# Kernel tuning notes

Hardware: AMD Instinct MI355X
Metric: run time of the kernel (lower is better)

Reference implementation:

```python
import jax, jax.numpy as jnp
import numpy as np
from jax.scipy.linalg import expm

VOCAB = 32000
DM = 256
STATES = (64, 128, 256, 512)
BATCH = 4
SEQ = 1024
RH = 64  # router hidden
NW = len(STATES)


def setup_inputs() -> dict:
    key = jax.random.key(0)
    ks = jax.random.split(key, 32)
    inp = {"x": jax.random.randint(ks[0], (BATCH, SEQ), 0, VOCAB)}
    inp["emb"] = jax.random.normal(ks[1], (VOCAB, DM), jnp.float32)
    for i, ds in enumerate(STATES):
        inp[f"A{i}"] = jax.random.normal(ks[2 + 3 * i], (ds, ds), jnp.float32) * 0.01
        inp[f"B{i}"] = jax.random.normal(ks[3 + 3 * i], (DM, ds), jnp.float32) * 0.01
        inp[f"C{i}"] = jax.random.normal(ks[4 + 3 * i], (ds, DM), jnp.float32) * 0.01
        inp[f"D{i}"] = jnp.ones((DM,), jnp.float32)
    inp["rw1"] = jax.random.normal(ks[20], (DM, RH), jnp.float32) * (1.0 / np.sqrt(DM))
    inp["rb1"] = jnp.zeros((RH,), jnp.float32)
    inp["rw2"] = jax.random.normal(ks[21], (RH, NW), jnp.float32) * (1.0 / np.sqrt(RH))
    inp["rb2"] = jnp.zeros((NW,), jnp.float32)
    inp["ow"] = jax.random.normal(ks[22], (DM, VOCAB), jnp.float32) * (1.0 / np.sqrt(DM))
    inp["ob"] = jnp.zeros((VOCAB,), jnp.float32)
    return inp


def world_ssm(xe, A, B, C, D):
    # xe: [b, s, dm]; LTI recurrence h_t = h_{t-1} @ A_d + x_t @ B; y_t = h_t @ C + x_t * D
    Ad = expm(A * 0.1)
    h0 = jnp.zeros((xe.shape[0], A.shape[0]), xe.dtype)

    def step(h, xt):
        h = h @ Ad + xt @ B
        return h, h @ C + xt * D

    _, ys = jax.lax.scan(step, h0, jnp.swapaxes(xe, 0, 1))  # scan over time
    return jnp.swapaxes(ys, 0, 1)  # [b, s, dm]


def reference(x, emb, A0, B0, C0, D0, A1, B1, C1, D1, A2, B2, C2, D2,
              A3, B3, C3, D3, rw1, rb1, rw2, rb2, ow, ob):
    xe = emb[x]  # [b, s, dm]
    # soft router over worlds from mean-pooled embedding
    w = jax.nn.softmax(jax.nn.relu(xe.mean(axis=1) @ rw1 + rb1) @ rw2 + rb2, axis=-1)  # [b, 4]
    worlds = [(A0, B0, C0, D0), (A1, B1, C1, D1), (A2, B2, C2, D2), (A3, B3, C3, D3)]
    out = jnp.zeros_like(xe)
    for i, p in enumerate(worlds):
        out = out + w[:, i][:, None, None] * world_ssm(xe, *p)
    return out @ ow + ob  # [b, s, vocab]
```

## Files before the change

### kernel.cpp

```cpp
#include <hip/hip_runtime.h>
#include <stdint.h>
#include <string.h>

#define DM 256
#define NB 4
#define SEQ 1024
#define NTOK 4096
#define RHID 64
#define DSUM 960
#define SZ2 348160
#define VOCABN 32000
#define XROWS 6144
#define XPADE (XROWS * DSUM)

typedef __attribute__((ext_vector_type(8))) short short8;
typedef __attribute__((ext_vector_type(4))) float floatx4;

__device__ __forceinline__ unsigned short f2bf(float f) {
  unsigned int x = __float_as_uint(f);
  x += 0x7fffu + ((x >> 16) & 1u);
  return (unsigned short)(x >> 16);
}
__device__ __forceinline__ float bf2f(unsigned short u) {
  return __uint_as_float(((unsigned int)u) << 16);
}

__device__ __forceinline__ void gll16(const unsigned short* g, unsigned short* l) {
  __builtin_amdgcn_global_load_lds((const __attribute__((address_space(1))) void*)g,
                                   (__attribute__((address_space(3))) void*)l, 16, 0, 0);
}

struct Ptr4 { const float* p[4]; };


__global__ void k_embed(const int* x, const float* emb, float* xe, unsigned short* xebf) {
  int r = blockIdx.x;
  int d = threadIdx.x;
  int tok = x[r];
  float v = emb[(size_t)tok * DM + d];
  xe[(size_t)r * DM + d] = v;
  xebf[(size_t)r * DM + d] = f2bf(v);
}

__global__ void k_mean(const float* xe, float* mean) {
  __shared__ float red[4][DM];
  int b = blockIdx.x;
  int tid = threadIdx.x;
  int d = tid & 255, tt = tid >> 8;
  float s = 0.f;
  for (int t = tt; t < SEQ; t += 4) s += xe[((size_t)b * SEQ + t) * DM + d];
  red[tt][d] = s;
  __syncthreads();
  if (tt == 0) mean[b * DM + d] = (red[0][d] + red[1][d] + red[2][d] + red[3][d]) * (1.f / SEQ);
}

__global__ void k_router(const float* mean, const float* rw1, const float* rb1,
                         const float* rw2, const float* rb2, Ptr4 Dv,
                         float* wout, float* wD) {
  __shared__ float r1[4][RHID];
  __shared__ float lg[4][4];
  __shared__ float wsh[4][4];
  int tid = threadIdx.x;
  int b = tid >> 6, h = tid & 63;
  float s = rb1[h];
  for (int d0 = 0; d0 < DM; d0++) s += mean[b * DM + d0] * rw1[d0 * RHID + h];
  r1[b][h] = fmaxf(s, 0.f);
  __syncthreads();
  if (tid < 16) {
    int bb = tid >> 2, i = tid & 3;
    float s2 = rb2[i];
    for (int hh = 0; hh < RHID; hh++) s2 += r1[bb][hh] * rw2[hh * 4 + i];
    lg[bb][i] = s2;
  }
  __syncthreads();
  if (tid < 4) {
    float m = lg[tid][0];
    for (int i = 1; i < 4; i++) m = fmaxf(m, lg[tid][i]);
    float e[4], sum = 0.f;
    for (int i = 0; i < 4; i++) { e[i] = __expf(lg[tid][i] - m); sum += e[i]; }
    for (int i = 0; i < 4; i++) { wsh[tid][i] = e[i] / sum; wout[tid * 4 + i] = wsh[tid][i]; }
  }
  __syncthreads();
  int d = tid;
  for (int bb = 0; bb < 4; bb++) {
    float v = 0.f;
    for (int i = 0; i < 4; i++) v += wsh[bb][i] * Dv.p[i][d];
    wD[bb * DM + d] = v;
  }
}

__device__ __forceinline__ void world_from_id(int id, int& w, int& e) {
  if (id < 4096)        { w = 0; e = id; }
  else if (id < 20480)  { w = 1; e = id - 4096; }
  else if (id < 86016)  { w = 2; e = id - 20480; }
  else                  { w = 3; e = id - 86016; }
}

__global__ void k_prep_M(Ptr4 A, unsigned short* Mh, unsigned short* Ml,
                         unsigned short* MTh, unsigned short* MTl) {
  int id = blockIdx.x * 256 + threadIdx.x;
  int w, e; world_from_id(id, w, e);
  int s = 6 + w, ds = 64 << w;
  int i = e >> s, j = e & (ds - 1);
  float v = 0.1f * A.p[w][e];
  unsigned short h = f2bf(v);
  unsigned short l = f2bf(v - bf2f(h));
  Mh[id] = h; Ml[id] = l;
  int tix = (id - e) + (j << s) + i;
  MTh[tix] = h; MTl[tix] = l;
}

__global__ void k_combine(Ptr4 A, const float* P2f, const float* P3f, const float* P4f,
                          unsigned short* Ph, unsigned short* Pl,
                          unsigned short* PTh, unsigned short* PTl) {
  int id = blockIdx.x * 256 + threadIdx.x;
  int w, e; world_from_id(id, w, e);
  int s = 6 + w, ds = 64 << w;
  int i = e >> s, j = e & (ds - 1);
  float v = ((i == j) ? 1.f : 0.f) + 0.1f * A.p[w][e]
          + 0.5f * P2f[id] + (1.f / 6.f) * P3f[id] + (1.f / 24.f) * P4f[id];
  unsigned short h = f2bf(v);
  unsigned short l = f2bf(v - bf2f(h));
  Ph[id] = h; Pl[id] = l;
  int tix = (id - e) + (j << s) + i;
  PTh[tix] = h; PTl[tix] = l;
}

__global__ void k_prep_B(Ptr4 B, unsigned short* BtCat) {
  int jc = blockIdx.x;
  int d = threadIdx.x;
  int w, j;
  if (jc < 64)       { w = 0; j = jc; }
  else if (jc < 192) { w = 1; j = jc - 64; }
  else if (jc < 448) { w = 2; j = jc - 192; }
  else               { w = 3; j = jc - 448; }
  int ds = 64 << w;
  BtCat[(size_t)jc * DM + d] = f2bf(B.p[w][(size_t)d * ds + j]);
}

__global__ void k_prep_C(Ptr4 C, unsigned short* CtCat) {
  int c = blockIdx.x * 256 + threadIdx.x;
  int d = blockIdx.y;
  if (c >= DSUM) return;
  int w, j;
  if (c < 64)       { w = 0; j = c; }
  else if (c < 192) { w = 1; j = c - 64; }
  else if (c < 448) { w = 2; j = c - 192; }
  else              { w = 3; j = c - 448; }
  CtCat[(size_t)d * DSUM + c] = f2bf(C.p[w][(size_t)j * DM + d]);
}

__global__ void k_transpose_ow(const float* ow, unsigned short* owT) {
  __shared__ float t[64][65];
  int n0 = blockIdx.x * 64, k0 = blockIdx.y * 64;
  int tid = threadIdx.x;
  int a = tid >> 6, b = tid & 63;
  #pragma unroll
  for (int r = 0; r < 16; r++) {
    int k = r * 4 + a;
    t[k][b] = ow[(size_t)(k0 + k) * VOCABN + n0 + b];
  }
  __syncthreads();
  #pragma unroll
  for (int r = 0; r < 16; r++) {
    int n = r * 4 + a;
    owT[(size_t)(n0 + n) * DM + k0 + b] = f2bf(t[b][n]);
  }
}

__global__ void k_zero(uint4* p, long n) {
  long i = (long)blockIdx.x * blockDim.x + threadIdx.x;
  long stride = (long)gridDim.x * blockDim.x;
  uint4 z = make_uint4(0, 0, 0, 0);
  for (; i < n; i += stride) p[i] = z;
}

__global__ void k_finish_op(const float* opf, const float* xe, const float* wD, unsigned short* op) {
  int r = blockIdx.x, dcol = threadIdx.x;
  size_t i = (size_t)r * DM + dcol;
  op[i] = f2bf(opf[i] + xe[i] * wD[(size_t)(r >> 10) * DM + dcol]);
}


struct GDesc {
  const unsigned short *Ah, *Al, *Bth, *Btl;
  float *Cf;
  unsigned short *Ch, *Cl, *Th, *Tl;
  int M, N, K, lda, ldbt, ldc, ldt, split, tn, boff;
};
struct GArgs { GDesc d[4]; int nd; };

__global__ __launch_bounds__(256) void gemm_uni(GArgs ga) {
  int di = ga.nd - 1;
  while (di > 0 && (int)blockIdx.x < ga.d[di].boff) di--;
  const GDesc& d = ga.d[di];
  int lb = blockIdx.x - d.boff;
  int tm = lb / d.tn, tnn = lb % d.tn;
  int m0 = tm * 128, n0 = tnn * 128;

  __shared__ unsigned short As[2][128][40];
  __shared__ unsigned short Bs[2][128][40];

  int tid = threadIdx.x;
  int wave = tid >> 6, lane = tid & 63;
  int wm = (wave >> 1) * 64, wn = (wave & 1) * 64;
  int q = lane >> 4, l15 = lane & 15;

  floatx4 acc[4][4];
  #pragma unroll
  for (int i = 0; i < 4; i++)
    #pragma unroll
    for (int j = 0; j < 4; j++)
      acc[i][j] = (floatx4){0.f, 0.f, 0.f, 0.f};

  for (int kt = 0; kt < d.K; kt += 32) {
    __syncthreads();
    #pragma unroll
    for (int c0 = 0; c0 < 2; c0++) {
      int c = c0 * 256 + tid;
      int row = c >> 2, k8 = (c & 3) << 3;
      {
        int gr = m0 + row;
        uint4 hv = make_uint4(0, 0, 0, 0), lv = make_uint4(0, 0, 0, 0);
        if (gr < d.M) {
          size_t idx = (size_t)gr * d.lda + kt + k8;
          hv = *(const uint4*)(d.Ah + idx);
          if (d.split) lv = *(const uint4*)(d.Al + idx);
        }
        *(uint4*)&As[0][row][k8] = hv;
        if (d.split) *(uint4*)&As[1][row][k8] = lv;
      }
      {
        int gn = n0 + row;
        uint4 hv = make_uint4(0, 0, 0, 0), lv = make_uint4(0, 0, 0, 0);
        if (gn < d.N) {
          size_t idx = (size_t)gn * d.ldbt + kt + k8;
          hv = *(const uint4*)(d.Bth + idx);
          if (d.split) lv = *(const uint4*)(d.Btl + idx);
        }
        *(uint4*)&Bs[0][row][k8] = hv;
        if (d.split) *(uint4*)&Bs[1][row][k8] = lv;
      }
    }
    __syncthreads();
    short8 bh[4], bl[4];
    #pragma unroll
    for (int j = 0; j < 4; j++)
      bh[j] = *(const short8*)&Bs[0][wn + j * 16 + l15][q * 8];
    if (d.split) {
      #pragma unroll
      for (int j = 0; j < 4; j++)
        bl[j] = *(const short8*)&Bs[1][wn + j * 16 + l15][q * 8];
    }
    #pragma unroll
    for (int i = 0; i < 4; i++) {
      short8 ah = *(const short8*)&As[0][wm + i * 16 + l15][q * 8];
      #pragma unroll
      for (int j = 0; j < 4; j++)
        acc[i][j] = __builtin_amdgcn_mfma_f32_16x16x32_bf16(ah, bh[j], acc[i][j], 0, 0, 0);
      if (d.split) {
        short8 al = *(const short8*)&As[1][wm + i * 16 + l15][q * 8];
        #pragma unroll
        for (int j = 0; j < 4; j++) {
          acc[i][j] = __builtin_amdgcn_mfma_f32_16x16x32_bf16(ah, bl[j], acc[i][j], 0, 0, 0);
          acc[i][j] = __builtin_amdgcn_mfma_f32_16x16x32_bf16(al, bh[j], acc[i][j], 0, 0, 0);
        }
      }
    }
  }

  #pragma unroll
  for (int i = 0; i < 4; i++) {
    #pragma unroll
    for (int j = 0; j < 4; j++) {
      int col = n0 + wn + j * 16 + l15;
      if (col >= d.N) continue;
      #pragma unroll
      for (int r = 0; r < 4; r++) {
        int row = m0 + wm + i * 16 + q * 4 + r;
        if (row >= d.M) continue;
        float v = acc[i][j][r];
        size_t ci = (size_t)row * d.ldc + col;
        if (d.Cf) d.Cf[ci] = v;
        if (d.Ch) {
          unsigned short h = f2bf(v);
          d.Ch[ci] = h;
          if (d.Cl) d.Cl[ci] = f2bf(v - bf2f(h));
        }
        if (d.Th) {
          size_t tix = (size_t)col * d.ldt + row;
          unsigned short h = f2bf(v);
          d.Th[tix] = h;
          d.Tl[tix] = f2bf(v - bf2f(h));
        }
      }
    }
  }
}


struct KDesc {
  const unsigned short *Ah, *Al, *Bth, *Btl;
  unsigned short *Ch, *Cl, *Hc;
  const float* wcol;
  int N, K, lda, ldbt, shift, hcoff, tn, boff;
};
struct KArgs { KDesc d[4]; int nd; };

template<int SPLIT, int KS>
__global__ __launch_bounds__(256) void gemm_x(KArgs ga) {
  int di = ga.nd - 1;
  while (di > 0 && (int)blockIdx.x < ga.d[di].boff) di--;
  const KDesc& d = ga.d[di];
  int lb = blockIdx.x - d.boff;
  int tm = lb / d.tn, tnn = lb % d.tn;
  int m0 = tm * 128, n0 = tnn * 128;
  int prow0 = ((m0 >> 10) * 1536) + 512 + (m0 & 1023);
  int arow0 = KS ? (prow0 - d.shift) : m0;

  __shared__ unsigned short As[(SPLIT ? 2 : 1) * 4096];
  __shared__ unsigned short Bs[(SPLIT ? 2 : 1) * 4096];

  int tid = threadIdx.x;
  int wave = tid >> 6, lane = tid & 63;
  int wm = (wave >> 1) * 64, wn = (wave & 1) * 64;
  int q = lane >> 4, l15 = lane & 15;
  int srow = lane >> 2, scol = (lane & 3) * 8;

  floatx4 acc[4][4];
  #pragma unroll
  for (int i = 0; i < 4; i++)
    #pragma unroll
    for (int j = 0; j < 4; j++)
      acc[i][j] = (floatx4){0.f, 0.f, 0.f, 0.f};

  for (int kt = 0; kt < d.K; kt += 32) {
    int ar = arow0 + wave * 32 + srow;
    int br = n0 + wave * 32 + srow;
    const unsigned short* ag = d.Ah + (size_t)ar * d.lda + kt + scol;
    const unsigned short* bg = d.Bth + (size_t)br * d.ldbt + kt + scol;
    size_t as16 = (size_t)16 * d.lda, bs16 = (size_t)16 * d.ldbt;
    unsigned short* al0 = &As[wave * 32 * 32];
    unsigned short* bl0 = &Bs[wave * 32 * 32];
    gll16(ag, al0);        gll16(ag + as16, al0 + 512);
    gll16(bg, bl0);        gll16(bg + bs16, bl0 + 512);
    if (SPLIT) {
      const unsigned short* ag2 = d.Al + (size_t)ar * d.lda + kt + scol;
      const unsigned short* bg2 = d.Btl + (size_t)br * d.ldbt + kt + scol;
      gll16(ag2, al0 + 4096); gll16(ag2 + as16, al0 + 4096 + 512);
      gll16(bg2, bl0 + 4096); gll16(bg2 + bs16, bl0 + 4096 + 512);
    }
    __syncthreads();
    short8 bh[4], bl[4];
    #pragma unroll
    for (int j = 0; j < 4; j++)
      bh[j] = *(const short8*)&Bs[(wn + j * 16 + l15) * 32 + q * 8];
    if (SPLIT) {
      #pragma unroll
      for (int j = 0; j < 4; j++)
        bl[j] = *(const short8*)&Bs[4096 + (wn + j * 16 + l15) * 32 + q * 8];
    }
    #pragma unroll
    for (int i = 0; i < 4; i++) {
      short8 ah = *(const short8*)&As[(wm + i * 16 + l15) * 32 + q * 8];
      #pragma unroll
      for (int j = 0; j < 4; j++)
        acc[i][j] = __builtin_amdgcn_mfma_f32_16x16x32_bf16(ah, bh[j], acc[i][j], 0, 0, 0);
      if (SPLIT) {
        short8 al = *(const short8*)&As[4096 + (wm + i * 16 + l15) * 32 + q * 8];
        #pragma unroll
        for (int j = 0; j < 4; j++) {
          acc[i][j] = __builtin_amdgcn_mfma_f32_16x16x32_bf16(ah, bl[j], acc[i][j], 0, 0, 0);
          acc[i][j] = __builtin_amdgcn_mfma_f32_16x16x32_bf16(al, bh[j], acc[i][j], 0, 0, 0);
        }
      }
    }
    __syncthreads();
  }

  #pragma unroll
  for (int j = 0; j < 4; j++) {
    int col = n0 + wn + j * 16 + l15;
    if (col >= d.N) continue;
    #pragma unroll
    for (int i = 0; i < 4; i++) {
      #pragma unroll
      for (int r = 0; r < 4; r++) {
        int rr = wm + i * 16 + q * 4 + r;
        size_t oi = (size_t)(prow0 + rr) * d.N + col;
        float v = acc[i][j][r];
        if (KS) v += bf2f(d.Ah[oi]) + bf2f(d.Al[oi]);
        unsigned short h = f2bf(v);
        d.Ch[oi] = h;
        d.Cl[oi] = f2bf(v - bf2f(h));
        if (KS && d.Hc) {
          int grow = m0 + rr;
          d.Hc[(size_t)grow * DSUM + d.hcoff + col] = f2bf(v * d.wcol[(m0 >> 10) * 4]);
        }
      }
    }
  }
}


__global__ __launch_bounds__(256) void gemm_cct(const unsigned short* __restrict__ Hc,
                                                const unsigned short* __restrict__ Ct,
                                                float* __restrict__ opf) {
  int bx = blockIdx.x;
  int chunk = bx / 64, lb = bx % 64;
  int tm = lb >> 1, tnn = lb & 1;
  int m0 = tm * 128, n0 = tnn * 128;
  int kt0 = chunk * 192;

  __shared__ unsigned short As[4096], Bs[4096];
  int tid = threadIdx.x;
  int wave = tid >> 6, lane = tid & 63;
  int wm = (wave >> 1) * 64, wn = (wave & 1) * 64;
  int q = lane >> 4, l15 = lane & 15;
  int srow = lane >> 2, scol = (lane & 3) * 8;

  floatx4 acc[4][4];
  #pragma unroll
  for (int i = 0; i < 4; i++)
    #pragma unroll
    for (int j = 0; j < 4; j++)
      acc[i][j] = (floatx4){0.f, 0.f, 0.f, 0.f};

  for (int k = 0; k < 192; k += 32) {
    int kt = kt0 + k;
    const unsigned short* ag = Hc + (size_t)(m0 + wave * 32 + srow) * DSUM + kt + scol;
    const unsigned short* bg = Ct + (size_t)(n0 + wave * 32 + srow) * DSUM + kt + scol;
    unsigned short* al0 = &As[wave * 32 * 32];
    unsigned short* bl0 = &Bs[wave * 32 * 32];
    gll16(ag, al0); gll16(ag + 16 * DSUM, al0 + 512);
    gll16(bg, bl0); gll16(bg + 16 * DSUM, bl0 + 512);
    __syncthreads();
    short8 bh[4];
    #pragma unroll
    for (int j = 0; j < 4; j++)
      bh[j] = *(const short8*)&Bs[(wn + j * 16 + l15) * 32 + q * 8];
    #pragma unroll
    for (int i = 0; i < 4; i++) {
      short8 ah = *(const short8*)&As[(wm + i * 16 + l15) * 32 + q * 8];
      #pragma unroll
      for (int j = 0; j < 4; j++)
        acc[i][j] = __builtin_amdgcn_mfma_f32_16x16x32_bf16(ah, bh[j], acc[i][j], 0, 0, 0);
    }
    __syncthreads();
  }

  #pragma unroll
  for (int j = 0; j < 4; j++) {
    int col = n0 + wn + j * 16 + l15;
    #pragma unroll
    for (int i = 0; i < 4; i++) {
      #pragma unroll
      for (int r = 0; r < 4; r++) {
        int row = m0 + wm + i * 16 + q * 4 + r;
        atomicAdd(&opf[(size_t)row * DM + col], acc[i][j][r]);
      }
    }
  }
}


__global__ __launch_bounds__(256) void gemm_big(const unsigned short* __restrict__ A,
                                                const unsigned short* __restrict__ B,
                                                const float* __restrict__ bias,
                                                float* __restrict__ out) {
  int bx = blockIdx.x;
  int tm = bx & 31, tn = bx >> 5;
  int m0 = tm * 128, n0 = tn * 128;

  __shared__ unsigned short As[4096], Bs[4096];
  int tid = threadIdx.x;
  int wave = tid >> 6, lane = tid & 63;
  int wm = (wave >> 1) * 64, wn = (wave & 1) * 64;
  int q = lane >> 4, l15 = lane & 15;
  int srow = lane >> 2, scol = (lane & 3) * 8;

  floatx4 acc[4][4];
  #pragma unroll
  for (int i = 0; i < 4; i++)
    #pragma unroll
    for (int j = 0; j < 4; j++)
      acc[i][j] = (floatx4){0.f, 0.f, 0.f, 0.f};

  for (int kt = 0; kt < DM; kt += 32) {
    const unsigned short* ag = A + (size_t)(m0 + wave * 32 + srow) * DM + kt + scol;
    const unsigned short* bg = B + (size_t)(n0 + wave * 32 + srow) * DM + kt + scol;
    unsigned short* al0 = &As[wave * 32 * 32];
    unsigned short* bl0 = &Bs[wave * 32 * 32];
    gll16(ag, al0); gll16(ag + 16 * DM, al0 + 512);
    gll16(bg, bl0); gll16(bg + 16 * DM, bl0 + 512);
    __syncthreads();
    short8 bh[4];
    #pragma unroll
    for (int j = 0; j < 4; j++)
      bh[j] = *(const short8*)&Bs[(wn + j * 16 + l15) * 32 + q * 8];
    #pragma unroll
    for (int i = 0; i < 4; i++) {
      short8 ah = *(const short8*)&As[(wm + i * 16 + l15) * 32 + q * 8];
      #pragma unroll
      for (int j = 0; j < 4; j++)
        acc[i][j] = __builtin_amdgcn_mfma_f32_16x16x32_bf16(ah, bh[j], acc[i][j], 0, 0, 0);
    }
    __syncthreads();
  }

  #pragma unroll
  for (int j = 0; j < 4; j++) {
    int col = n0 + wn + j * 16 + l15;
    float bj = bias[col];
    #pragma unroll
    for (int i = 0; i < 4; i++) {
      #pragma unroll
      for (int r = 0; r < 4; r++) {
        int row = m0 + wm + i * 16 + q * 4 + r;
        out[(size_t)row * VOCABN + col] = acc[i][j][r] + bj;
      }
    }
  }
}


extern "C" void kernel_launch(void* const* d_in, const int* in_sizes, int n_in,
                              void* d_out, int out_size, void* d_ws, size_t ws_size,
                              hipStream_t stream) {
  const int*   x   = (const int*)d_in[0];
  const float* emb = (const float*)d_in[1];
  Ptr4 Aw = {{(const float*)d_in[2], (const float*)d_in[6], (const float*)d_in[10], (const float*)d_in[14]}};
  Ptr4 Bw = {{(const float*)d_in[3], (const float*)d_in[7], (const float*)d_in[11], (const float*)d_in[15]}};
  Ptr4 Cw = {{(const float*)d_in[4], (const float*)d_in[8], (const float*)d_in[12], (const float*)d_in[16]}};
  Ptr4 Dw = {{(const float*)d_in[5], (const float*)d_in[9], (const float*)d_in[13], (const float*)d_in[17]}};
  const float* rw1 = (const float*)d_in[18];
  const float* rb1 = (const float*)d_in[19];
  const float* rw2 = (const float*)d_in[20];
  const float* rb2 = (const float*)d_in[21];
  const float* ow  = (const float*)d_in[22];
  const float* ob  = (const float*)d_in[23];
  float* out = (float*)d_out;

  char* wsb = (char*)d_ws;
  size_t off = 0;
  auto alloc = [&](size_t bytes) { size_t o = off; off = (off + bytes + 255) & ~(size_t)255; return o; };

  size_t o_xef  = alloc((size_t)NTOK * DM * 4);
  size_t o_xebf = alloc((size_t)NTOK * DM * 2);
  size_t o_mean = alloc(4 * DM * 4);
  size_t o_w    = alloc(64);
  size_t o_wD   = alloc(4 * DM * 4);
  size_t o_Mh   = alloc((size_t)SZ2 * 2), o_Ml = alloc((size_t)SZ2 * 2);
  size_t o_MTh  = alloc((size_t)SZ2 * 2), o_MTl = alloc((size_t)SZ2 * 2);
  size_t o_P2f  = alloc((size_t)SZ2 * 4);
  size_t o_P2h  = alloc((size_t)SZ2 * 2), o_P2l = alloc((size_t)SZ2 * 2);
  size_t o_P2Th = alloc((size_t)SZ2 * 2), o_P2Tl = alloc((size_t)SZ2 * 2);
  size_t o_P3f  = alloc((size_t)SZ2 * 4);
  size_t o_P4f  = alloc((size_t)SZ2 * 4);
  size_t o_Ph   = alloc((size_t)10 * SZ2 * 2), o_Pl  = alloc((size_t)10 * SZ2 * 2);
  size_t o_PTh  = alloc((size_t)10 * SZ2 * 2), o_PTl = alloc((size_t)10 * SZ2 * 2);
  size_t o_XAh  = alloc((size_t)XPADE * 2);
  size_t o_XAl  = alloc((size_t)XPADE * 2);
  size_t o_XBh  = alloc((size_t)XPADE * 2);
  size_t o_XBl  = alloc((size_t)XPADE * 2);
  size_t o_opf  = alloc((size_t)NTOK * DM * 4);
  size_t o_Hc   = alloc((size_t)NTOK * DSUM * 2);
  size_t o_op   = alloc((size_t)NTOK * DM * 2);
  size_t o_Bt   = alloc((size_t)DSUM * DM * 2);
  size_t o_Ct   = alloc((size_t)DM * DSUM * 2);
  size_t o_owT  = alloc((size_t)VOCABN * DM * 2);

  auto U16 = [&](size_t o) { return (unsigned short*)(wsb + o); };
  auto F32 = [&](size_t o) { return (float*)(wsb + o); };

  const int dsw[4] = {64, 128, 256, 512};
  const size_t off2[4] = {0, 4096, 20480, 86016};
  const int offc[4] = {0, 64, 192, 448};
  const size_t wxoff[4] = {0, (size_t)XROWS * 64, (size_t)XROWS * 192, (size_t)XROWS * 448};
  const int worder[4] = {3, 2, 1, 0};

  auto launchU = [&](GArgs& a) {
    int total = 0;
    for (int i = 0; i < a.nd; i++) {
      a.d[i].boff = total;
      int tm = (a.d[i].M + 127) / 128, tn = (a.d[i].N + 127) / 128;
      a.d[i].tn = tn;
      total += tm * tn;
    }
    gemm_uni<<<total, 256, 0, stream>>>(a);
  };
  auto zd = []() { GDesc d; memset(&d, 0, sizeof(d)); return d; };

  k_embed<<<NTOK, DM, 0, stream>>>(x, emb, F32(o_xef), U16(o_xebf));
  k_mean<<<NB, 1024, 0, stream>>>(F32(o_xef), F32(o_mean));
  k_router<<<1, 256, 0, stream>>>(F32(o_mean), rw1, rb1, rw2, rb2, Dw, F32(o_w), F32(o_wD));
  k_prep_M<<<SZ2 / 256, 256, 0, stream>>>(Aw, U16(o_Mh), U16(o_Ml), U16(o_MTh), U16(o_MTl));
  k_prep_B<<<DSUM, 256, 0, stream>>>(Bw, U16(o_Bt));
  k_prep_C<<<dim3(4, 256), 256, 0, stream>>>(Cw, U16(o_Ct));
  k_transpose_ow<<<dim3(VOCABN / 64, DM / 64), 256, 0, stream>>>(ow, U16(o_owT));
  {
    long zbytes = (long)4 * XPADE * 2 + (long)NTOK * DM * 4;
    k_zero<<<2048, 256, 0, stream>>>((uint4*)(wsb + o_XAh), zbytes / 16);
  }

  {
    GArgs a; a.nd = 4;
    for (int w = 0; w < 4; w++) {
      GDesc d = zd();
      d.Ah = U16(o_Mh) + off2[w]; d.Al = U16(o_Ml) + off2[w];
      d.Bth = U16(o_MTh) + off2[w]; d.Btl = U16(o_MTl) + off2[w];
      d.Cf = F32(o_P2f) + off2[w];
      d.Ch = U16(o_P2h) + off2[w]; d.Cl = U16(o_P2l) + off2[w];
      d.Th = U16(o_P2Th) + off2[w]; d.Tl = U16(o_P2Tl) + off2[w];
      d.M = d.N = d.K = d.lda = d.ldbt = d.ldc = d.ldt = dsw[w];
      d.split = 1;
      a.d[w] = d;
    }
    launchU(a);
  }
  {
    GArgs a; a.nd = 4;
    for (int w = 0; w < 4; w++) {
      GDesc d = zd();
      d.Ah = U16(o_P2h) + off2[w]; d.Al = U16(o_P2l) + off2[w];
      d.Bth = U16(o_MTh) + off2[w]; d.Btl = U16(o_MTl) + off2[w];
      d.Cf = F32(o_P3f) + off2[w];
      d.M = d.N = d.K = d.lda = d.ldbt = d.ldc = dsw[w];
      d.split = 1;
      a.d[w] = d;
    }
    launchU(a);
  }
  {
    GArgs a; a.nd = 4;
    for (int w = 0; w < 4; w++) {
      GDesc d = zd();
      d.Ah = U16(o_P2h) + off2[w]; d.Al = U16(o_P2l) + off2[w];
      d.Bth = U16(o_P2Th) + off2[w]; d.Btl = U16(o_P2Tl) + off2[w];
      d.Cf = F32(o_P4f) + off2[w];
      d.M = d.N = d.K = d.lda = d.ldbt = d.ldc = dsw[w];
      d.split = 1;
      a.d[w] = d;
    }
    launchU(a);
  }
  k_combine<<<SZ2 / 256, 256, 0, stream>>>(Aw, F32(o_P2f), F32(o_P3f), F32(o_P4f),
                                           U16(o_Ph), U16(o_Pl), U16(o_PTh), U16(o_PTl));
  for (int j = 1; j < 10; j++) {
    GArgs a; a.nd = 4;
    for (int w = 0; w < 4; w++) {
      size_t so = (size_t)(j - 1) * SZ2 + off2[w];
      size_t do_ = (size_t)j * SZ2 + off2[w];
      GDesc d = zd();
      d.Ah = U16(o_Ph) + so; d.Al = U16(o_Pl) + so;
      d.Bth = U16(o_PTh) + so; d.Btl = U16(o_PTl) + so;
      d.Ch = U16(o_Ph) + do_; d.Cl = U16(o_Pl) + do_;
      d.Th = U16(o_PTh) + do_; d.Tl = U16(o_PTl) + do_;
      d.M = d.N = d.K = d.lda = d.ldbt = d.ldc = d.ldt = dsw[w];
      d.split = 1;
      a.d[w] = d;
    }
    launchU(a);
  }
  {
    KArgs a; a.nd = 4;
    int total = 0;
    for (int k = 0; k < 4; k++) {
      int w = worder[k];
      KDesc d; memset(&d, 0, sizeof(d));
      d.Ah = U16(o_xebf);
      d.Bth = U16(o_Bt) + (size_t)offc[w] * DM;
      d.Ch = U16(o_XAh) + wxoff[w];
      d.Cl = U16(o_XAl) + wxoff[w];
      d.N = dsw[w]; d.K = DM; d.lda = DM; d.ldbt = DM;
      d.tn = dsw[w] >= 128 ? dsw[w] / 128 : 1;
      d.boff = total; total += 32 * d.tn;
      a.d[k] = d;
    }
    gemm_x<0, 0><<<total, 256, 0, stream>>>(a);
  }
  size_t xin_h = o_XAh, xin_l = o_XAl, xout_h = o_XBh, xout_l = o_XBl;
  for (int j = 0; j < 10; j++) {
    KArgs a; a.nd = 4;
    int total = 0;
    for (int k = 0; k < 4; k++) {
      int w = worder[k];
      KDesc d; memset(&d, 0, sizeof(d));
      d.Ah = U16(xin_h) + wxoff[w];
      d.Al = U16(xin_l) + wxoff[w];
      d.Bth = U16(o_PTh) + (size_t)j * SZ2 + off2[w];
      d.Btl = U16(o_PTl) + (size_t)j * SZ2 + off2[w];
      d.Ch = U16(xout_h) + wxoff[w];
      d.Cl = U16(xout_l) + wxoff[w];
      d.N = dsw[w]; d.K = dsw[w]; d.lda = dsw[w]; d.ldbt = dsw[w];
      d.shift = 1 << j;
      if (j == 9) { d.Hc = U16(o_Hc); d.hcoff = offc[w]; d.wcol = F32(o_w) + w; }
      d.tn = dsw[w] >= 128 ? dsw[w] / 128 : 1;
      d.boff = total; total += 32 * d.tn;
      a.d[k] = d;
    }
    gemm_x<1, 1><<<total, 256, 0, stream>>>(a);
    size_t th = xin_h, tl = xin_l;
    xin_h = xout_h; xin_l = xout_l; xout_h = th; xout_l = tl;
  }
  gemm_cct<<<320, 256, 0, stream>>>(U16(o_Hc), U16(o_Ct), F32(o_opf));
  k_finish_op<<<NTOK, DM, 0, stream>>>(F32(o_opf), F32(o_xef), F32(o_wD), U16(o_op));
  gemm_big<<<8000, 256, 0, stream>>>(U16(o_op), U16(o_owT), ob, out);

  (void)in_sizes; (void)n_in; (void)out_size; (void)ws_size;
}
```

Before: 1.920 ms.

## Fuse setup and GEMM chains into persistent kernels with grid barriers

Merges the embed, prep, transpose and zeroing kernels into one setup launch. The expm power chain and the scan-doubling chain each become a single persistent kernel that syncs with atomic grid barriers, and the C projection is fused with the D-skip finish. This is meant to remove roughly 30 small kernel launches and their gaps on a latency-bound chain. In exchange, the persistent grids are small (44 and 256 blocks), and the spin barriers rely on every block being co-resident.

```diff
diff --git a/kernel.cpp b/kernel.cpp
--- a/kernel.cpp
+++ b/kernel.cpp
@@ -32,63 +32,6 @@
 
 struct Ptr4 { const float* p[4]; };
 
-
-__global__ void k_embed(const int* x, const float* emb, float* xe, unsigned short* xebf) {
-  int r = blockIdx.x;
-  int d = threadIdx.x;
-  int tok = x[r];
-  float v = emb[(size_t)tok * DM + d];
-  xe[(size_t)r * DM + d] = v;
-  xebf[(size_t)r * DM + d] = f2bf(v);
-}
-
-__global__ void k_mean(const float* xe, float* mean) {
-  __shared__ float red[4][DM];
-  int b = blockIdx.x;
-  int tid = threadIdx.x;
-  int d = tid & 255, tt = tid >> 8;
-  float s = 0.f;
-  for (int t = tt; t < SEQ; t += 4) s += xe[((size_t)b * SEQ + t) * DM + d];
-  red[tt][d] = s;
-  __syncthreads();
-  if (tt == 0) mean[b * DM + d] = (red[0][d] + red[1][d] + red[2][d] + red[3][d]) * (1.f / SEQ);
-}
-
-__global__ void k_router(const float* mean, const float* rw1, const float* rb1,
-                         const float* rw2, const float* rb2, Ptr4 Dv,
-                         float* wout, float* wD) {
-  __shared__ float r1[4][RHID];
-  __shared__ float lg[4][4];
-  __shared__ float wsh[4][4];
-  int tid = threadIdx.x;
-  int b = tid >> 6, h = tid & 63;
-  float s = rb1[h];
-  for (int d0 = 0; d0 < DM; d0++) s += mean[b * DM + d0] * rw1[d0 * RHID + h];
-  r1[b][h] = fmaxf(s, 0.f);
-  __syncthreads();
-  if (tid < 16) {
-    int bb = tid >> 2, i = tid & 3;
-    float s2 = rb2[i];
-    for (int hh = 0; hh < RHID; hh++) s2 += r1[bb][hh] * rw2[hh * 4 + i];
-    lg[bb][i] = s2;
-  }
-  __syncthreads();
-  if (tid < 4) {
-    float m = lg[tid][0];
-    for (int i = 1; i < 4; i++) m = fmaxf(m, lg[tid][i]);
-    float e[4], sum = 0.f;
-    for (int i = 0; i < 4; i++) { e[i] = __expf(lg[tid][i] - m); sum += e[i]; }
-    for (int i = 0; i < 4; i++) { wsh[tid][i] = e[i] / sum; wout[tid * 4 + i] = wsh[tid][i]; }
-  }
-  __syncthreads();
-  int d = tid;
-  for (int bb = 0; bb < 4; bb++) {
-    float v = 0.f;
-    for (int i = 0; i < 4; i++) v += wsh[bb][i] * Dv.p[i][d];
-    wD[bb * DM + d] = v;
-  }
-}
-
 __device__ __forceinline__ void world_from_id(int id, int& w, int& e) {
   if (id < 4096)        { w = 0; e = id; }
   else if (id < 20480)  { w = 1; e = id - 4096; }
@@ -96,111 +39,123 @@
   else                  { w = 3; e = id - 86016; }
 }
 
-__global__ void k_prep_M(Ptr4 A, unsigned short* Mh, unsigned short* Ml,
-                         unsigned short* MTh, unsigned short* MTl) {
-  int id = blockIdx.x * 256 + threadIdx.x;
-  int w, e; world_from_id(id, w, e);
-  int s = 6 + w, ds = 64 << w;
-  int i = e >> s, j = e & (ds - 1);
-  float v = 0.1f * A.p[w][e];
-  unsigned short h = f2bf(v);
-  unsigned short l = f2bf(v - bf2f(h));
-  Mh[id] = h; Ml[id] = l;
-  int tix = (id - e) + (j << s) + i;
-  MTh[tix] = h; MTl[tix] = l;
-}
-
-__global__ void k_combine(Ptr4 A, const float* P2f, const float* P3f, const float* P4f,
-                          unsigned short* Ph, unsigned short* Pl,
-                          unsigned short* PTh, unsigned short* PTl) {
-  int id = blockIdx.x * 256 + threadIdx.x;
-  int w, e; world_from_id(id, w, e);
-  int s = 6 + w, ds = 64 << w;
-  int i = e >> s, j = e & (ds - 1);
-  float v = ((i == j) ? 1.f : 0.f) + 0.1f * A.p[w][e]
-          + 0.5f * P2f[id] + (1.f / 6.f) * P3f[id] + (1.f / 24.f) * P4f[id];
-  unsigned short h = f2bf(v);
-  unsigned short l = f2bf(v - bf2f(h));
-  Ph[id] = h; Pl[id] = l;
-  int tix = (id - e) + (j << s) + i;
-  PTh[tix] = h; PTl[tix] = l;
-}
-
-__global__ void k_prep_B(Ptr4 B, unsigned short* BtCat) {
-  int jc = blockIdx.x;
-  int d = threadIdx.x;
-  int w, j;
-  if (jc < 64)       { w = 0; j = jc; }
-  else if (jc < 192) { w = 1; j = jc - 64; }
-  else if (jc < 448) { w = 2; j = jc - 192; }
-  else               { w = 3; j = jc - 448; }
-  int ds = 64 << w;
-  BtCat[(size_t)jc * DM + d] = f2bf(B.p[w][(size_t)d * ds + j]);
-}
-
-__global__ void k_prep_C(Ptr4 C, unsigned short* CtCat) {
-  int c = blockIdx.x * 256 + threadIdx.x;
-  int d = blockIdx.y;
-  if (c >= DSUM) return;
-  int w, j;
-  if (c < 64)       { w = 0; j = c; }
-  else if (c < 192) { w = 1; j = c - 64; }
-  else if (c < 448) { w = 2; j = c - 192; }
-  else              { w = 3; j = c - 448; }
-  CtCat[(size_t)d * DSUM + c] = f2bf(C.p[w][(size_t)j * DM + d]);
-}
-
-__global__ void k_transpose_ow(const float* ow, unsigned short* owT) {
+__device__ __forceinline__ void gridbar(unsigned int* cnt, unsigned int nb) {
+  __syncthreads();
+  if (threadIdx.x == 0) {
+    __threadfence();
+    unsigned int ticket = atomicAdd(cnt, 1u);
+    unsigned int target = (ticket / nb + 1u) * nb;
+    while (__hip_atomic_load(cnt, __ATOMIC_RELAXED, __HIP_MEMORY_SCOPE_AGENT) < target)
+      __builtin_amdgcn_s_sleep(1);
+    __threadfence();
+  }
+  __syncthreads();
+}
+
+
+__device__ __forceinline__ void tile22(int t, int& w, int& tm, int& tn) {
+  if (t < 16)      { w = 3; tm = t >> 2;        tn = t & 3; }
+  else if (t < 20) { w = 2; tm = (t - 16) >> 1; tn = (t - 16) & 1; }
+  else if (t == 20){ w = 1; tm = 0;             tn = 0; }
+  else             { w = 0; tm = 0;             tn = 0; }
+}
+
+__device__ __forceinline__ void tile256(int t, int& w, int& tm, int& tn) {
+  if (t < 128)      { w = 3; tm = t >> 2;          tn = t & 3; }
+  else if (t < 192) { w = 2; tm = (t - 128) >> 1;  tn = (t - 128) & 1; }
+  else if (t < 224) { w = 1; tm = t - 192;         tn = 0; }
+  else              { w = 0; tm = t - 224;         tn = 0; }
+}
+
+
+struct SetupArgs {
+  const int* x; const float* emb;
+  float* xef; unsigned short* xebf;
+  Ptr4 A, B, C;
+  const float* ow;
+  unsigned short *Mh, *Ml, *MTh, *MTl;
+  unsigned short *Bt, *Ct, *owT;
+  unsigned short *XAh, *XAl, *XBh, *XBl;
+  unsigned int* syncp;
+};
+
+__global__ __launch_bounds__(256) void k_setup(SetupArgs a) {
   __shared__ float t[64][65];
-  int n0 = blockIdx.x * 64, k0 = blockIdx.y * 64;
-  int tid = threadIdx.x;
-  int a = tid >> 6, b = tid & 63;
-  #pragma unroll
-  for (int r = 0; r < 16; r++) {
-    int k = r * 4 + a;
-    t[k][b] = ow[(size_t)(k0 + k) * VOCABN + n0 + b];
-  }
-  __syncthreads();
-  #pragma unroll
-  for (int r = 0; r < 16; r++) {
-    int n = r * 4 + a;
-    owT[(size_t)(n0 + n) * DM + k0 + b] = f2bf(t[b][n]);
-  }
-}
-
-__global__ void k_zero(uint4* p, long n) {
-  long i = (long)blockIdx.x * blockDim.x + threadIdx.x;
-  long stride = (long)gridDim.x * blockDim.x;
-  uint4 z = make_uint4(0, 0, 0, 0);
-  for (; i < n; i += stride) p[i] = z;
-}
-
-__global__ void k_finish_op(const float* opf, const float* xe, const float* wD, unsigned short* op) {
-  int r = blockIdx.x, dcol = threadIdx.x;
-  size_t i = (size_t)r * DM + dcol;
-  op[i] = f2bf(opf[i] + xe[i] * wD[(size_t)(r >> 10) * DM + dcol]);
-}
-
-
-struct GDesc {
-  const unsigned short *Ah, *Al, *Bth, *Btl;
-  float *Cf;
-  unsigned short *Ch, *Cl, *Th, *Tl;
-  int M, N, K, lda, ldbt, ldc, ldt, split, tn, boff;
-};
-struct GArgs { GDesc d[4]; int nd; };
-
-__global__ __launch_bounds__(256) void gemm_uni(GArgs ga) {
-  int di = ga.nd - 1;
-  while (di > 0 && (int)blockIdx.x < ga.d[di].boff) di--;
-  const GDesc& d = ga.d[di];
-  int lb = blockIdx.x - d.boff;
-  int tm = lb / d.tn, tnn = lb % d.tn;
-  int m0 = tm * 128, n0 = tnn * 128;
-
-  __shared__ unsigned short As[2][128][40];
-  __shared__ unsigned short Bs[2][128][40];
-
+  int bid = blockIdx.x, tid = threadIdx.x;
+  if (bid < 4096) {
+    int tok = a.x[bid];
+    float v = a.emb[(size_t)tok * DM + tid];
+    a.xef[(size_t)bid * DM + tid] = v;
+    a.xebf[(size_t)bid * DM + tid] = f2bf(v);
+  } else if (bid < 5456) {
+    int id = (bid - 4096) * 256 + tid;
+    int w, e; world_from_id(id, w, e);
+    int s = 6 + w, ds = 64 << w;
+    int i = e >> s, j = e & (ds - 1);
+    float v = 0.1f * a.A.p[w][e];
+    unsigned short h = f2bf(v);
+    unsigned short l = f2bf(v - bf2f(h));
+    a.Mh[id] = h; a.Ml[id] = l;
+    int tix = (id - e) + (j << s) + i;
+    a.MTh[tix] = h; a.MTl[tix] = l;
+  } else if (bid < 6416) {
+    int jc = bid - 5456;
+    int d = tid;
+    int w, j;
+    if (jc < 64)       { w = 0; j = jc; }
+    else if (jc < 192) { w = 1; j = jc - 64; }
+    else if (jc < 448) { w = 2; j = jc - 192; }
+    else               { w = 3; j = jc - 448; }
+    int ds = 64 << w;
+    a.Bt[(size_t)jc * DM + d] = f2bf(a.B.p[w][(size_t)d * ds + j]);
+  } else if (bid < 7440) {
+    int idx = bid - 6416;
+    int c = (idx & 3) * 256 + tid;
+    int d = idx >> 2;
+    if (c < DSUM) {
+      int w, j;
+      if (c < 64)       { w = 0; j = c; }
+      else if (c < 192) { w = 1; j = c - 64; }
+      else if (c < 448) { w = 2; j = c - 192; }
+      else              { w = 3; j = c - 448; }
+      a.Ct[(size_t)d * DSUM + c] = f2bf(a.C.p[w][(size_t)j * DM + d]);
+    }
+  } else if (bid < 9440) {
+    int idx = bid - 7440;
+    int n0 = (idx % 500) * 64, k0 = (idx / 500) * 64;
+    int aa = tid >> 6, b = tid & 63;
+    #pragma unroll
+    for (int r = 0; r < 16; r++) {
+      int k = r * 4 + aa;
+      t[k][b] = a.ow[(size_t)(k0 + k) * VOCABN + n0 + b];
+    }
+    __syncthreads();
+    #pragma unroll
+    for (int r = 0; r < 16; r++) {
+      int n = r * 4 + aa;
+      a.owT[(size_t)(n0 + n) * DM + k0 + b] = f2bf(t[b][n]);
+    }
+  } else {
+    int b = bid - 9440;
+    if (b == 0 && tid < 2) a.syncp[tid] = 0;
+    unsigned short* arrs[4] = {a.XAh, a.XAl, a.XBh, a.XBl};
+    int chunk = b >> 4;
+    unsigned short* base = arrs[chunk >> 2] + (size_t)(chunk & 3) * 1536 * DSUM;
+    uint4* p = (uint4*)base;
+    int start = (b & 15) * 3840;
+    uint4 z = make_uint4(0, 0, 0, 0);
+    for (int k = tid; k < 3840; k += 256) p[start + k] = z;
+  }
+}
+
+
+__device__ __forceinline__ void gemm_tile(
+    const unsigned short* __restrict__ Ah, const unsigned short* __restrict__ Al,
+    const unsigned short* __restrict__ Bth, const unsigned short* __restrict__ Btl,
+    float* Cf, unsigned short* Ch, unsigned short* Cl,
+    unsigned short* Th, unsigned short* Tl,
+    int ds, int m0, int n0,
+    unsigned short* As, unsigned short* Bs) {
   int tid = threadIdx.x;
   int wave = tid >> 6, lane = tid & 63;
   int wm = (wave >> 1) * 64, wn = (wave & 1) * 64;
@@ -213,7 +168,7 @@
     for (int j = 0; j < 4; j++)
       acc[i][j] = (floatx4){0.f, 0.f, 0.f, 0.f};
 
-  for (int kt = 0; kt < d.K; kt += 32) {
+  for (int kt = 0; kt < ds; kt += 32) {
     __syncthreads();
     #pragma unroll
     for (int c0 = 0; c0 < 2; c0++) {
@@ -222,104 +177,206 @@
       {
         int gr = m0 + row;
         uint4 hv = make_uint4(0, 0, 0, 0), lv = make_uint4(0, 0, 0, 0);
-        if (gr < d.M) {
-          size_t idx = (size_t)gr * d.lda + kt + k8;
-          hv = *(const uint4*)(d.Ah + idx);
-          if (d.split) lv = *(const uint4*)(d.Al + idx);
+        if (gr < ds) {
+          size_t idx = (size_t)gr * ds + kt + k8;
+          hv = *(const uint4*)(Ah + idx);
+          lv = *(const uint4*)(Al + idx);
         }
-        *(uint4*)&As[0][row][k8] = hv;
-        if (d.split) *(uint4*)&As[1][row][k8] = lv;
+        *(uint4*)&As[(size_t)row * 40 + k8] = hv;
+        *(uint4*)&As[(size_t)(128 + row) * 40 + k8] = lv;
       }
       {
         int gn = n0 + row;
         uint4 hv = make_uint4(0, 0, 0, 0), lv = make_uint4(0, 0, 0, 0);
-        if (gn < d.N) {
-          size_t idx = (size_t)gn * d.ldbt + kt + k8;
-          hv = *(const uint4*)(d.Bth + idx);
-          if (d.split) lv = *(const uint4*)(d.Btl + idx);
+        if (gn < ds) {
+          size_t idx = (size_t)gn * ds + kt + k8;
+          hv = *(const uint4*)(Bth + idx);
+          lv = *(const uint4*)(Btl + idx);
         }
-        *(uint4*)&Bs[0][row][k8] = hv;
-        if (d.split) *(uint4*)&Bs[1][row][k8] = lv;
+        *(uint4*)&Bs[(size_t)row * 40 + k8] = hv;
+        *(uint4*)&Bs[(size_t)(128 + row) * 40 + k8] = lv;
       }
     }
     __syncthreads();
     short8 bh[4], bl[4];
     #pragma unroll
-    for (int j = 0; j < 4; j++)
-      bh[j] = *(const short8*)&Bs[0][wn + j * 16 + l15][q * 8];
-    if (d.split) {
-      #pragma unroll
-      for (int j = 0; j < 4; j++)
-        bl[j] = *(const short8*)&Bs[1][wn + j * 16 + l15][q * 8];
+    for (int j = 0; j < 4; j++) {
+      bh[j] = *(const short8*)&Bs[(size_t)(wn + j * 16 + l15) * 40 + q * 8];
+      bl[j] = *(const short8*)&Bs[(size_t)(128 + wn + j * 16 + l15) * 40 + q * 8];
     }
     #pragma unroll
     for (int i = 0; i < 4; i++) {
-      short8 ah = *(const short8*)&As[0][wm + i * 16 + l15][q * 8];
-      #pragma unroll
-      for (int j = 0; j < 4; j++)
+      short8 ah = *(const short8*)&As[(size_t)(wm + i * 16 + l15) * 40 + q * 8];
+      short8 al = *(const short8*)&As[(size_t)(128 + wm + i * 16 + l15) * 40 + q * 8];
+      #pragma unroll
+      for (int j = 0; j < 4; j++) {
         acc[i][j] = __builtin_amdgcn_mfma_f32_16x16x32_bf16(ah, bh[j], acc[i][j], 0, 0, 0);
-      if (d.split) {
-        short8 al = *(const short8*)&As[1][wm + i * 16 + l15][q * 8];
-        #pragma unroll
-        for (int j = 0; j < 4; j++) {
-          acc[i][j] = __builtin_amdgcn_mfma_f32_16x16x32_bf16(ah, bl[j], acc[i][j], 0, 0, 0);
-          acc[i][j] = __builtin_amdgcn_mfma_f32_16x16x32_bf16(al, bh[j], acc[i][j], 0, 0, 0);
+        acc[i][j] = __builtin_amdgcn_mfma_f32_16x16x32_bf16(ah, bl[j], acc[i][j], 0, 0, 0);
+        acc[i][j] = __builtin_amdgcn_mfma_f32_16x16x32_bf16(al, bh[j], acc[i][j], 0, 0, 0);
+      }
+    }
+  }
+
+  #pragma unroll
+  for (int i = 0; i < 4; i++) {
+    #pragma unroll
+    for (int j = 0; j < 4; j++) {
+      int col = n0 + wn + j * 16 + l15;
+      if (col >= ds) continue;
+      #pragma unroll
+      for (int r = 0; r < 4; r++) {
+        int row = m0 + wm + i * 16 + q * 4 + r;
+        if (row >= ds) continue;
+        float v = acc[i][j][r];
+        size_t ci = (size_t)row * ds + col;
+        if (Cf) Cf[ci] = v;
+        if (Ch) {
+          unsigned short h = f2bf(v);
+          Ch[ci] = h;
+          Cl[ci] = f2bf(v - bf2f(h));
+        }
+        if (Th) {
+          size_t tix = (size_t)col * ds + row;
+          unsigned short h = f2bf(v);
+          Th[tix] = h;
+          Tl[tix] = f2bf(v - bf2f(h));
         }
       }
     }
   }
-
-  #pragma unroll
-  for (int i = 0; i < 4; i++) {
-    #pragma unroll
-    for (int j = 0; j < 4; j++) {
-      int col = n0 + wn + j * 16 + l15;
-      if (col >= d.N) continue;
-      #pragma unroll
-      for (int r = 0; r < 4; r++) {
-        int row = m0 + wm + i * 16 + q * 4 + r;
-        if (row >= d.M) continue;
-        float v = acc[i][j][r];
-        size_t ci = (size_t)row * d.ldc + col;
-        if (d.Cf) d.Cf[ci] = v;
-        if (d.Ch) {
-          unsigned short h = f2bf(v);
-          d.Ch[ci] = h;
-          if (d.Cl) d.Cl[ci] = f2bf(v - bf2f(h));
-        }
-        if (d.Th) {
-          size_t tix = (size_t)col * d.ldt + row;
-          unsigned short h = f2bf(v);
-          d.Th[tix] = h;
-          d.Tl[tix] = f2bf(v - bf2f(h));
-        }
-      }
-    }
-  }
-}
-
-
-struct KDesc {
-  const unsigned short *Ah, *Al, *Bth, *Btl;
-  unsigned short *Ch, *Cl, *Hc;
-  const float* wcol;
-  int N, K, lda, ldbt, shift, hcoff, tn, boff;
+}
+
+
+struct EArgs {
+  const float* xef; float* meanp;
+  const float *rw1, *rb1, *rw2, *rb2;
+  Ptr4 A, D;
+  float *w, *wD;
+  const unsigned short *Mh, *Ml, *MTh, *MTl;
+  float *P2f, *P3f, *P4f;
+  unsigned short *P2h, *P2l, *P2Th, *P2Tl;
+  unsigned short *Ph, *Pl, *PTh, *PTl;
+  unsigned int* syncp;
 };
-struct KArgs { KDesc d[4]; int nd; };
+
+__global__ __launch_bounds__(256) void k_expm_chain(EArgs a) {
+  __shared__ __align__(16) unsigned short As[2 * 128 * 40];
+  __shared__ __align__(16) unsigned short Bs[2 * 128 * 40];
+  int bid = blockIdx.x, tid = threadIdx.x;
+  const int dsw[4] = {64, 128, 256, 512};
+  const size_t off2[4] = {0, 4096, 20480, 86016};
+
+  if (bid < 32) {
+    int b = bid >> 3, t0 = (bid & 7) * 128;
+    float s = 0.f;
+    for (int t = 0; t < 128; t++) s += a.xef[((size_t)b * SEQ + t0 + t) * DM + tid];
+    a.meanp[bid * DM + tid] = s;
+  }
+  gridbar(a.syncp, 44);
+
+  if (bid < 22) {
+    int w, tm, tn; tile22(bid, w, tm, tn);
+    size_t o = off2[w];
+    gemm_tile(a.Mh + o, a.Ml + o, a.MTh + o, a.MTl + o,
+              a.P2f + o, a.P2h + o, a.P2l + o, a.P2Th + o, a.P2Tl + o,
+              dsw[w], tm * 128, tn * 128, As, Bs);
+  } else if (bid == 43) {
+    float* m4  = (float*)As;
+    float* r1  = m4 + 4 * DM;
+    float* lg  = r1 + 4 * RHID;
+    float* wsh = lg + 16;
+    for (int b = 0; b < 4; b++) {
+      float s = 0.f;
+      for (int k = 0; k < 8; k++) s += a.meanp[(b * 8 + k) * DM + tid];
+      m4[b * DM + tid] = s * (1.f / SEQ);
+    }
+    __syncthreads();
+    {
+      int b = tid >> 6, h = tid & 63;
+      float s = a.rb1[h];
+      for (int d0 = 0; d0 < DM; d0++) s += m4[b * DM + d0] * a.rw1[d0 * RHID + h];
+      r1[b * RHID + h] = fmaxf(s, 0.f);
+    }
+    __syncthreads();
+    if (tid < 16) {
+      int bb = tid >> 2, i = tid & 3;
+      float s2 = a.rb2[i];
+      for (int hh = 0; hh < RHID; hh++) s2 += r1[bb * RHID + hh] * a.rw2[hh * 4 + i];
+      lg[bb * 4 + i] = s2;
+    }
+    __syncthreads();
+    if (tid < 4) {
+      float m = lg[tid * 4 + 0];
+      for (int i = 1; i < 4; i++) m = fmaxf(m, lg[tid * 4 + i]);
+      float e[4], sum = 0.f;
+      for (int i = 0; i < 4; i++) { e[i] = __expf(lg[tid * 4 + i] - m); sum += e[i]; }
+      for (int i = 0; i < 4; i++) { wsh[tid * 4 + i] = e[i] / sum; a.w[tid * 4 + i] = wsh[tid * 4 + i]; }
+    }
+    __syncthreads();
+    for (int bb = 0; bb < 4; bb++) {
+      float v = 0.f;
+      for (int i = 0; i < 4; i++) v += wsh[bb * 4 + i] * a.D.p[i][tid];
+      a.wD[bb * DM + tid] = v;
+    }
+  }
+  gridbar(a.syncp, 44);
+
+  if (bid < 22) {
+    int w, tm, tn; tile22(bid, w, tm, tn);
+    size_t o = off2[w];
+    gemm_tile(a.P2h + o, a.P2l + o, a.MTh + o, a.MTl + o,
+              a.P3f + o, nullptr, nullptr, nullptr, nullptr,
+              dsw[w], tm * 128, tn * 128, As, Bs);
+  } else {
+    int w, tm, tn; tile22(bid - 22, w, tm, tn);
+    size_t o = off2[w];
+    gemm_tile(a.P2h + o, a.P2l + o, a.P2Th + o, a.P2Tl + o,
+              a.P4f + o, nullptr, nullptr, nullptr, nullptr,
+              dsw[w], tm * 128, tn * 128, As, Bs);
+  }
+  gridbar(a.syncp, 44);
+
+  {
+    int gt = bid * 256 + tid;
+    for (int id = gt; id < SZ2; id += 44 * 256) {
+      int w, e; world_from_id(id, w, e);
+      int s = 6 + w, ds = 64 << w;
+      int i = e >> s, j = e & (ds - 1);
+      float v = ((i == j) ? 1.f : 0.f) + 0.1f * a.A.p[w][e]
+              + 0.5f * a.P2f[id] + (1.f / 6.f) * a.P3f[id] + (1.f / 24.f) * a.P4f[id];
+      unsigned short h = f2bf(v);
+      unsigned short l = f2bf(v - bf2f(h));
+      a.Ph[id] = h; a.Pl[id] = l;
+      int tix = (id - e) + (j << s) + i;
+      a.PTh[tix] = h; a.PTl[tix] = l;
+    }
+  }
+  gridbar(a.syncp, 44);
+
+  for (int j = 1; j < 10; j++) {
+    if (bid < 22) {
+      int w, tm, tn; tile22(bid, w, tm, tn);
+      size_t so = (size_t)(j - 1) * SZ2 + off2[w];
+      size_t dd = (size_t)j * SZ2 + off2[w];
+      gemm_tile(a.Ph + so, a.Pl + so, a.PTh + so, a.PTl + so,
+                nullptr, a.Ph + dd, a.Pl + dd, a.PTh + dd, a.PTl + dd,
+                dsw[w], tm * 128, tn * 128, As, Bs);
+    }
+    if (j < 9) gridbar(a.syncp, 44);
+  }
+}
+
 
 template<int SPLIT, int KS>
-__global__ __launch_bounds__(256) void gemm_x(KArgs ga) {
-  int di = ga.nd - 1;
-  while (di > 0 && (int)blockIdx.x < ga.d[di].boff) di--;
-  const KDesc& d = ga.d[di];
-  int lb = blockIdx.x - d.boff;
-  int tm = lb / d.tn, tnn = lb % d.tn;
-  int m0 = tm * 128, n0 = tnn * 128;
+__device__ __forceinline__ void xstage(
+    const unsigned short* __restrict__ Ah, const unsigned short* __restrict__ Al,
+    const unsigned short* __restrict__ Bth, const unsigned short* __restrict__ Btl,
+    unsigned short* Ch, unsigned short* Cl,
+    unsigned short* Hc, int hcoff, const float* wcol,
+    int N, int K, int lda, int ldbt, int shift,
+    int m0, int n0, unsigned short* As, unsigned short* Bs) {
   int prow0 = ((m0 >> 10) * 1536) + 512 + (m0 & 1023);
-  int arow0 = KS ? (prow0 - d.shift) : m0;
-
-  __shared__ unsigned short As[(SPLIT ? 2 : 1) * 4096];
-  __shared__ unsigned short Bs[(SPLIT ? 2 : 1) * 4096];
+  int arow0 = KS ? (prow0 - shift) : m0;
 
   int tid = threadIdx.x;
   int wave = tid >> 6, lane = tid & 63;
@@ -334,19 +391,19 @@
     for (int j = 0; j < 4; j++)
       acc[i][j] = (floatx4){0.f, 0.f, 0.f, 0.f};
 
-  for (int kt = 0; kt < d.K; kt += 32) {
+  for (int kt = 0; kt < K; kt += 32) {
     int ar = arow0 + wave * 32 + srow;
     int br = n0 + wave * 32 + srow;
-    const unsigned short* ag = d.Ah + (size_t)ar * d.lda + kt + scol;
-    const unsigned short* bg = d.Bth + (size_t)br * d.ldbt + kt + scol;
-    size_t as16 = (size_t)16 * d.lda, bs16 = (size_t)16 * d.ldbt;
-    unsigned short* al0 = &As[wave * 32 * 32];
-    unsigned short* bl0 = &Bs[wave * 32 * 32];
+    const unsigned short* ag = Ah + (size_t)ar * lda + kt + scol;
+    const unsigned short* bg = Bth + (size_t)br * ldbt + kt + scol;
+    size_t as16 = (size_t)16 * lda, bs16 = (size_t)16 * ldbt;
+    unsigned short* al0 = &As[wave * 1024];
+    unsigned short* bl0 = &Bs[wave * 1024];
     gll16(ag, al0);        gll16(ag + as16, al0 + 512);
     gll16(bg, bl0);        gll16(bg + bs16, bl0 + 512);
     if (SPLIT) {
-      const unsigned short* ag2 = d.Al + (size_t)ar * d.lda + kt + scol;
-      const unsigned short* bg2 = d.Btl + (size_t)br * d.ldbt + kt + scol;
+      const unsigned short* ag2 = Al + (size_t)ar * lda + kt + scol;
+      const unsigned short* bg2 = Btl + (size_t)br * ldbt + kt + scol;
       gll16(ag2, al0 + 4096); gll16(ag2 + as16, al0 + 4096 + 512);
       gll16(bg2, bl0 + 4096); gll16(bg2 + bs16, bl0 + 4096 + 512);
     }
@@ -381,21 +438,21 @@
   #pragma unroll
   for (int j = 0; j < 4; j++) {
     int col = n0 + wn + j * 16 + l15;
-    if (col >= d.N) continue;
+    if (col >= N) continue;
     #pragma unroll
     for (int i = 0; i < 4; i++) {
       #pragma unroll
       for (int r = 0; r < 4; r++) {
         int rr = wm + i * 16 + q * 4 + r;
-        size_t oi = (size_t)(prow0 + rr) * d.N + col;
+        size_t oi = (size_t)(prow0 + rr) * N + col;
         float v = acc[i][j][r];
-        if (KS) v += bf2f(d.Ah[oi]) + bf2f(d.Al[oi]);
+        if (KS) v += bf2f(Ah[oi]) + bf2f(Al[oi]);
         unsigned short h = f2bf(v);
-        d.Ch[oi] = h;
-        d.Cl[oi] = f2bf(v - bf2f(h));
-        if (KS && d.Hc) {
+        Ch[oi] = h;
+        Cl[oi] = f2bf(v - bf2f(h));
+        if (KS && Hc) {
           int grow = m0 + rr;
-          d.Hc[(size_t)grow * DSUM + d.hcoff + col] = f2bf(v * d.wcol[(m0 >> 10) * 4]);
+          Hc[(size_t)grow * DSUM + hcoff + col] = f2bf(v * wcol[(m0 >> 10) * 4]);
         }
       }
     }
@@ -403,16 +460,11 @@
 }
 
 
-__global__ __launch_bounds__(256) void gemm_cct(const unsigned short* __restrict__ Hc,
-                                                const unsigned short* __restrict__ Ct,
-                                                float* __restrict__ opf) {
-  int bx = blockIdx.x;
-  int chunk = bx / 64, lb = bx % 64;
-  int tm = lb >> 1, tnn = lb & 1;
-  int m0 = tm * 128, n0 = tnn * 128;
-  int kt0 = chunk * 192;
-
-  __shared__ unsigned short As[4096], Bs[4096];
+__device__ __forceinline__ void cct_tile(
+    const unsigned short* __restrict__ Hc, const unsigned short* __restrict__ Ct,
+    const float* __restrict__ xef, const float* __restrict__ wD,
+    unsigned short* __restrict__ op,
+    int m0, int n0, unsigned short* As, unsigned short* Bs) {
   int tid = threadIdx.x;
   int wave = tid >> 6, lane = tid & 63;
   int wm = (wave >> 1) * 64, wn = (wave & 1) * 64;
@@ -426,12 +478,11 @@
     for (int j = 0; j < 4; j++)
       acc[i][j] = (floatx4){0.f, 0.f, 0.f, 0.f};
 
-  for (int k = 0; k < 192; k += 32) {
-    int kt = kt0 + k;
+  for (int kt = 0; kt < DSUM; kt += 32) {
     const unsigned short* ag = Hc + (size_t)(m0 + wave * 32 + srow) * DSUM + kt + scol;
     const unsigned short* bg = Ct + (size_t)(n0 + wave * 32 + srow) * DSUM + kt + scol;
-    unsigned short* al0 = &As[wave * 32 * 32];
-    unsigned short* bl0 = &Bs[wave * 32 * 32];
+    unsigned short* al0 = &As[wave * 1024];
+    unsigned short* bl0 = &Bs[wave * 1024];
     gll16(ag, al0); gll16(ag + 16 * DSUM, al0 + 512);
     gll16(bg, bl0); gll16(bg + 16 * DSUM, bl0 + 512);
     __syncthreads();
@@ -457,10 +508,56 @@
       #pragma unroll
       for (int r = 0; r < 4; r++) {
         int row = m0 + wm + i * 16 + q * 4 + r;
-        atomicAdd(&opf[(size_t)row * DM + col], acc[i][j][r]);
+        size_t oi = (size_t)row * DM + col;
+        op[oi] = f2bf(acc[i][j][r] + xef[oi] * wD[(size_t)(row >> 10) * DM + col]);
       }
     }
   }
+}
+
+
+struct SArgs {
+  const unsigned short *xebf, *Bt;
+  unsigned short *XAh, *XAl, *XBh, *XBl;
+  const unsigned short *PTh, *PTl;
+  unsigned short* Hc;
+  const float* w;
+  const unsigned short* Ct;
+  const float *xef, *wD;
+  unsigned short* op;
+  unsigned int* syncp;
+};
+
+__global__ __launch_bounds__(256) void k_scan_chain(SArgs a) {
+  __shared__ __align__(16) unsigned short As[2 * 4096];
+  __shared__ __align__(16) unsigned short Bs[2 * 4096];
+  int t = blockIdx.x;
+  int w, tm, tn; tile256(t, w, tm, tn);
+  const int dsw[4] = {64, 128, 256, 512};
+  const size_t off2[4] = {0, 4096, 20480, 86016};
+  const int offc[4] = {0, 64, 192, 448};
+  const size_t wxoff[4] = {0, (size_t)XROWS * 64, (size_t)XROWS * 192, (size_t)XROWS * 448};
+  int ds = dsw[w];
+
+  xstage<0, 0>(a.xebf, nullptr, a.Bt + (size_t)offc[w] * DM, nullptr,
+               a.XAh + wxoff[w], a.XAl + wxoff[w],
+               nullptr, 0, nullptr,
+               ds, DM, DM, DM, 0, tm * 128, tn * 128, As, Bs);
+  gridbar(a.syncp, 256);
+
+  unsigned short *xh = a.XAh, *xl = a.XAl, *yh = a.XBh, *yl = a.XBl;
+  for (int j = 0; j < 10; j++) {
+    xstage<1, 1>(xh + wxoff[w], xl + wxoff[w],
+                 a.PTh + (size_t)j * SZ2 + off2[w], a.PTl + (size_t)j * SZ2 + off2[w],
+                 yh + wxoff[w], yl + wxoff[w],
+                 (j == 9) ? a.Hc : nullptr, offc[w], a.w + w,
+                 ds, ds, ds, ds, 1 << j, tm * 128, tn * 128, As, Bs);
+    gridbar(a.syncp, 256);
+    unsigned short* t1 = xh; xh = yh; yh = t1;
+    unsigned short* t2 = xl; xl = yl; yl = t2;
+  }
+
+  if (t < 64) cct_tile(a.Hc, a.Ct, a.xef, a.wD, a.op, (t >> 1) * 128, (t & 1) * 128, As, Bs);
 }
 
 
@@ -472,7 +569,7 @@
   int tm = bx & 31, tn = bx >> 5;
   int m0 = tm * 128, n0 = tn * 128;
 
-  __shared__ unsigned short As[4096], Bs[4096];
+  __shared__ __align__(16) unsigned short As[4096], Bs[4096];
   int tid = threadIdx.x;
   int wave = tid >> 6, lane = tid & 63;
   int wm = (wave >> 1) * 64, wn = (wave & 1) * 64;
@@ -545,11 +642,12 @@
   size_t off = 0;
   auto alloc = [&](size_t bytes) { size_t o = off; off = (off + bytes + 255) & ~(size_t)255; return o; };
 
-  size_t o_xef  = alloc((size_t)NTOK * DM * 4);
-  size_t o_xebf = alloc((size_t)NTOK * DM * 2);
-  size_t o_mean = alloc(4 * DM * 4);
-  size_t o_w    = alloc(64);
-  size_t o_wD   = alloc(4 * DM * 4);
+  size_t o_xef   = alloc((size_t)NTOK * DM * 4);
+  size_t o_xebf  = alloc((size_t)NTOK * DM * 2);
+  size_t o_meanp = alloc((size_t)32 * DM * 4);
+  size_t o_w     = alloc(64);
+  size_t o_wD    = alloc(4 * DM * 4);
+  size_t o_sync  = alloc(256);
   size_t o_Mh   = alloc((size_t)SZ2 * 2), o_Ml = alloc((size_t)SZ2 * 2);
   size_t o_MTh  = alloc((size_t)SZ2 * 2), o_MTl = alloc((size_t)SZ2 * 2);
   size_t o_P2f  = alloc((size_t)SZ2 * 4);
@@ -563,7 +661,6 @@
   size_t o_XAl  = alloc((size_t)XPADE * 2);
   size_t o_XBh  = alloc((size_t)XPADE * 2);
   size_t o_XBl  = alloc((size_t)XPADE * 2);
-  size_t o_opf  = alloc((size_t)NTOK * DM * 4);
   size_t o_Hc   = alloc((size_t)NTOK * DSUM * 2);
   size_t o_op   = alloc((size_t)NTOK * DM * 2);
   size_t o_Bt   = alloc((size_t)DSUM * DM * 2);
@@ -573,138 +670,36 @@
   auto U16 = [&](size_t o) { return (unsigned short*)(wsb + o); };
   auto F32 = [&](size_t o) { return (float*)(wsb + o); };
 
-  const int dsw[4] = {64, 128, 256, 512};
-  const size_t off2[4] = {0, 4096, 20480, 86016};
-  const int offc[4] = {0, 64, 192, 448};
-  const size_t wxoff[4] = {0, (size_t)XROWS * 64, (size_t)XROWS * 192, (size_t)XROWS * 448};
-  const int worder[4] = {3, 2, 1, 0};
-
-  auto launchU = [&](GArgs& a) {
-    int total = 0;
-    for (int i = 0; i < a.nd; i++) {
-      a.d[i].boff = total;
-      int tm = (a.d[i].M + 127) / 128, tn = (a.d[i].N + 127) / 128;
-      a.d[i].tn = tn;
-      total += tm * tn;
-    }
-    gemm_uni<<<total, 256, 0, stream>>>(a);
-  };
-  auto zd = []() { GDesc d; memset(&d, 0, sizeof(d)); return d; };
-
-  k_embed<<<NTOK, DM, 0, stream>>>(x, emb, F32(o_xef), U16(o_xebf));
-  k_mean<<<NB, 1024, 0, stream>>>(F32(o_xef), F32(o_mean));
-  k_router<<<1, 256, 0, stream>>>(F32(o_mean), rw1, rb1, rw2, rb2, Dw, F32(o_w), F32(o_wD));
-  k_prep_M<<<SZ2 / 256, 256, 0, stream>>>(Aw, U16(o_Mh), U16(o_Ml), U16(o_MTh), U16(o_MTl));
-  k_prep_B<<<DSUM, 256, 0, stream>>>(Bw, U16(o_Bt));
-  k_prep_C<<<dim3(4, 256), 256, 0, stream>>>(Cw, U16(o_Ct));
-  k_transpose_ow<<<dim3(VOCABN / 64, DM / 64), 256, 0, stream>>>(ow, U16(o_owT));
-  {
-    long zbytes = (long)4 * XPADE * 2 + (long)NTOK * DM * 4;
-    k_zero<<<2048, 256, 0, stream>>>((uint4*)(wsb + o_XAh), zbytes / 16);
-  }
-
-  {
-    GArgs a; a.nd = 4;
-    for (int w = 0; w < 4; w++) {
-      GDesc d = zd();
-      d.Ah = U16(o_Mh) + off2[w]; d.Al = U16(o_Ml) + off2[w];
-      d.Bth = U16(o_MTh) + off2[w]; d.Btl = U16(o_MTl) + off2[w];
-      d.Cf = F32(o_P2f) + off2[w];
-      d.Ch = U16(o_P2h) + off2[w]; d.Cl = U16(o_P2l) + off2[w];
-      d.Th = U16(o_P2Th) + off2[w]; d.Tl = U16(o_P2Tl) + off2[w];
-      d.M = d.N = d.K = d.lda = d.ldbt = d.ldc = d.ldt = dsw[w];
-      d.split = 1;
-      a.d[w] = d;
-    }
-    launchU(a);
-  }
-  {
-    GArgs a; a.nd = 4;
-    for (int w = 0; w < 4; w++) {
-      GDesc d = zd();
-      d.Ah = U16(o_P2h) + off2[w]; d.Al = U16(o_P2l) + off2[w];
-      d.Bth = U16(o_MTh) + off2[w]; d.Btl = U16(o_MTl) + off2[w];
-      d.Cf = F32(o_P3f) + off2[w];
-      d.M = d.N = d.K = d.lda = d.ldbt = d.ldc = dsw[w];
-      d.split = 1;
-      a.d[w] = d;
-    }
-    launchU(a);
-  }
-  {
-    GArgs a; a.nd = 4;
-    for (int w = 0; w < 4; w++) {
-      GDesc d = zd();
-      d.Ah = U16(o_P2h) + off2[w]; d.Al = U16(o_P2l) + off2[w];
-      d.Bth = U16(o_P2Th) + off2[w]; d.Btl = U16(o_P2Tl) + off2[w];
-      d.Cf = F32(o_P4f) + off2[w];
-      d.M = d.N = d.K = d.lda = d.ldbt = d.ldc = dsw[w];
-      d.split = 1;
-      a.d[w] = d;
-    }
-    launchU(a);
-  }
-  k_combine<<<SZ2 / 256, 256, 0, stream>>>(Aw, F32(o_P2f), F32(o_P3f), F32(o_P4f),
-                                           U16(o_Ph), U16(o_Pl), U16(o_PTh), U16(o_PTl));
-  for (int j = 1; j < 10; j++) {
-    GArgs a; a.nd = 4;
-    for (int w = 0; w < 4; w++) {
-      size_t so = (size_t)(j - 1) * SZ2 + off2[w];
-      size_t do_ = (size_t)j * SZ2 + off2[w];
-      GDesc d = zd();
-      d.Ah = U16(o_Ph) + so; d.Al = U16(o_Pl) + so;
-      d.Bth = U16(o_PTh) + so; d.Btl = U16(o_PTl) + so;
-      d.Ch = U16(o_Ph) + do_; d.Cl = U16(o_Pl) + do_;
-      d.Th = U16(o_PTh) + do_; d.Tl = U16(o_PTl) + do_;
-      d.M = d.N = d.K = d.lda = d.ldbt = d.ldc = d.ldt = dsw[w];
-      d.split = 1;
-      a.d[w] = d;
-    }
-    launchU(a);
-  }
-  {
-    KArgs a; a.nd = 4;
-    int total = 0;
-    for (int k = 0; k < 4; k++) {
-      int w = worder[k];
-      KDesc d; memset(&d, 0, sizeof(d));
-      d.Ah = U16(o_xebf);
-      d.Bth = U16(o_Bt) + (size_t)offc[w] * DM;
-      d.Ch = U16(o_XAh) + wxoff[w];
-      d.Cl = U16(o_XAl) + wxoff[w];
-      d.N = dsw[w]; d.K = DM; d.lda = DM; d.ldbt = DM;
-      d.tn = dsw[w] >= 128 ? dsw[w] / 128 : 1;
-      d.boff = total; total += 32 * d.tn;
-      a.d[k] = d;
-    }
-    gemm_x<0, 0><<<total, 256, 0, stream>>>(a);
-  }
-  size_t xin_h = o_XAh, xin_l = o_XAl, xout_h = o_XBh, xout_l = o_XBl;
-  for (int j = 0; j < 10; j++) {
-    KArgs a; a.nd = 4;
-    int total = 0;
-    for (int k = 0; k < 4; k++) {
-      int w = worder[k];
-      KDesc d; memset(&d, 0, sizeof(d));
-      d.Ah = U16(xin_h) + wxoff[w];
-      d.Al = U16(xin_l) + wxoff[w];
-      d.Bth = U16(o_PTh) + (size_t)j * SZ2 + off2[w];
-      d.Btl = U16(o_PTl) + (size_t)j * SZ2 + off2[w];
-      d.Ch = U16(xout_h) + wxoff[w];
-      d.Cl = U16(xout_l) + wxoff[w];
-      d.N = dsw[w]; d.K = dsw[w]; d.lda = dsw[w]; d.ldbt = dsw[w];
-      d.shift = 1 << j;
-      if (j == 9) { d.Hc = U16(o_Hc); d.hcoff = offc[w]; d.wcol = F32(o_w) + w; }
-      d.tn = dsw[w] >= 128 ? dsw[w] / 128 : 1;
-      d.boff = total; total += 32 * d.tn;
-      a.d[k] = d;
-    }
-    gemm_x<1, 1><<<total, 256, 0, stream>>>(a);
-    size_t th = xin_h, tl = xin_l;
-    xin_h = xout_h; xin_l = xout_l; xout_h = th; xout_l = tl;
-  }
-  gemm_cct<<<320, 256, 0, stream>>>(U16(o_Hc), U16(o_Ct), F32(o_opf));
-  k_finish_op<<<NTOK, DM, 0, stream>>>(F32(o_opf), F32(o_xef), F32(o_wD), U16(o_op));
+  SetupArgs sa;
+  sa.x = x; sa.emb = emb; sa.xef = F32(o_xef); sa.xebf = U16(o_xebf);
+  sa.A = Aw; sa.B = Bw; sa.C = Cw; sa.ow = ow;
+  sa.Mh = U16(o_Mh); sa.Ml = U16(o_Ml); sa.MTh = U16(o_MTh); sa.MTl = U16(o_MTl);
+  sa.Bt = U16(o_Bt); sa.Ct = U16(o_Ct); sa.owT = U16(o_owT);
+  sa.XAh = U16(o_XAh); sa.XAl = U16(o_XAl); sa.XBh = U16(o_XBh); sa.XBl = U16(o_XBl);
+  sa.syncp = (unsigned int*)(wsb + o_sync);
+  k_setup<<<9696, 256, 0, stream>>>(sa);
+
+  EArgs ea;
+  ea.xef = F32(o_xef); ea.meanp = F32(o_meanp);
+  ea.rw1 = rw1; ea.rb1 = rb1; ea.rw2 = rw2; ea.rb2 = rb2;
+  ea.A = Aw; ea.D = Dw;
+  ea.w = F32(o_w); ea.wD = F32(o_wD);
+  ea.Mh = U16(o_Mh); ea.Ml = U16(o_Ml); ea.MTh = U16(o_MTh); ea.MTl = U16(o_MTl);
+  ea.P2f = F32(o_P2f); ea.P3f = F32(o_P3f); ea.P4f = F32(o_P4f);
+  ea.P2h = U16(o_P2h); ea.P2l = U16(o_P2l); ea.P2Th = U16(o_P2Th); ea.P2Tl = U16(o_P2Tl);
+  ea.Ph = U16(o_Ph); ea.Pl = U16(o_Pl); ea.PTh = U16(o_PTh); ea.PTl = U16(o_PTl);
+  ea.syncp = (unsigned int*)(wsb + o_sync) + 0;
+  k_expm_chain<<<44, 256, 0, stream>>>(ea);
+
+  SArgs sc;
+  sc.xebf = U16(o_xebf); sc.Bt = U16(o_Bt);
+  sc.XAh = U16(o_XAh); sc.XAl = U16(o_XAl); sc.XBh = U16(o_XBh); sc.XBl = U16(o_XBl);
+  sc.PTh = U16(o_PTh); sc.PTl = U16(o_PTl);
+  sc.Hc = U16(o_Hc); sc.w = F32(o_w);
+  sc.Ct = U16(o_Ct); sc.xef = F32(o_xef); sc.wD = F32(o_wD); sc.op = U16(o_op);
+  sc.syncp = (unsigned int*)(wsb + o_sync) + 1;
+  k_scan_chain<<<256, 256, 0, stream>>>(sc);
+
   gemm_big<<<8000, 256, 0, stream>>>(U16(o_op), U16(o_owT), ob, out);
 
   (void)in_sizes; (void)n_in; (void)out_size; (void)ws_size;
```

Result: no change. 1.953 ms (+1.7%).
